# Kernel optimization log

Measured on AMD Instinct MI355X. Metric: run time of the kernel, lower is better.

Reference implementation:

```python
import jax, jax.numpy as jnp
import numpy as np

H = 16      # num_attention_heads
D = 64      # attention_head_size
HID = H * D # hidden_size = 1024
N = 1024    # seq_len == max_len
K = 1024    # position_buckets == att_span (K >= N so un-clamped indices stay in range)
EPS = 1e-7  # layer_norm_eps


def setup_inputs() -> dict:
    key = jax.random.key(0)
    ks = jax.random.split(key, 12)

    def w(k, shape):
        return jax.random.normal(k, shape, dtype=jnp.float32) * 0.02

    return {
        "hidden_states": jax.random.normal(ks[0], (1, N, HID), dtype=jnp.float32),
        "rel_embeddings": jax.random.normal(ks[1], (2 * K, HID), dtype=jnp.float32),
        "Wq": w(ks[2], (HID, HID)), "bq": jnp.zeros((HID,), jnp.float32),
        "Wk": w(ks[3], (HID, HID)), "bk": jnp.zeros((HID,), jnp.float32),
        "Wv": w(ks[4], (HID, HID)), "bv": jnp.zeros((HID,), jnp.float32),
        "Wpk": w(ks[5], (HID, HID)), "bpk": jnp.zeros((HID,), jnp.float32),
        "Wpq": w(ks[6], (HID, HID)), "bpq": jnp.zeros((HID,), jnp.float32),
        "Wo": w(ks[7], (HID, HID)), "bo": jnp.zeros((HID,), jnp.float32),
        "ln_g": jnp.ones((HID,), jnp.float32),
        "ln_b": jnp.zeros((HID,), jnp.float32),
    }


def _heads(x):
    # (L, HID) -> (H, L, D)   (batch size is 1, matching the baked-in id offsets)
    L = x.shape[0]
    return x.reshape(L, H, D).transpose(1, 0, 2)


def reference(hidden_states, rel_embeddings, Wq, bq, Wk, bk, Wv, bv,
              Wpk, bpk, Wpq, bpq, Wo, bo, ln_g, ln_b):
    hs = hidden_states[0]                       # (N, HID)
    q = _heads(hs @ Wq.T + bq)                  # (H, N, D)
    k = _heads(hs @ Wk.T + bk)                  # (H, N, D)
    v = _heads(hs @ Wv.T + bv)                  # (H, N, D)

    scale = jnp.sqrt(jnp.asarray(D * 3, jnp.float32))  # scale_factor = 1 + c2p + p2c = 3
    scores = jnp.einsum('hid,hjd->hij', q, k) / scale  # (H, N, N)

    pos_k = _heads(rel_embeddings @ Wpk.T + bpk)       # (H, 2K, D)
    pos_q = _heads(rel_embeddings @ Wpq.T + bpq)       # (H, 2K, D)

    rows = jnp.arange(N)[:, None]                      # (N, 1)
    # ids[i, j] = (i - j) + K  (no clamp in the original; valid since K >= N)
    idx = K + jnp.arange(N)[:, None] - jnp.arange(N)[None, :]  # (N, N)

    # c2p: gather c2p_att[h, i, K + i - j]
    c2p_att = jnp.einsum('hid,hkd->hik', q, pos_k)     # (H, N, 2K)
    c2p = c2p_att[:, rows, idx]                        # (H, N, N)

    # p2c: gather p2c_att[h, i, K + j - i], then transpose last two dims
    p2c_att = jnp.einsum('hid,hkd->hik', k, pos_q)     # (H, N, 2K)
    p2c = jnp.swapaxes(p2c_att[:, rows, idx.T], -1, -2)  # (H, N, N)

    scores = scores + (c2p + p2c) / scale
    attn = jax.nn.softmax(scores, axis=-1)             # (H, N, N)

    ctx = jnp.einsum('hij,hjd->hid', attn, v)          # (H, N, D)
    ctx = ctx.transpose(1, 0, 2).reshape(1, N, HID)    # (1, N, HID)

    # DebertaV2SelfOutput: dense + residual LayerNorm
    out = ctx @ Wo.T + bo
    x = out + hidden_states
    mu = jnp.mean(x, axis=-1, keepdims=True)
    var = jnp.mean(jnp.square(x - mu), axis=-1, keepdims=True)
    return ((x - mu) / jnp.sqrt(var + EPS)) * ln_g + ln_b
```

## Files before the change

### kernel.cpp

```cpp
#include <hip/hip_runtime.h>
#include <stdint.h>

#define HID 1024
#define NSEQ 1024
#define KREL 1024
#define NHEAD 16
#define DHEAD 64

typedef __attribute__((ext_vector_type(8))) short bhalf8;
typedef __attribute__((ext_vector_type(4))) float floatx4;

__device__ inline uint16_t f2bf(float f) {
  union { float f; uint32_t u; } c; c.f = f;
  uint32_t u = c.u;
  return (uint16_t)((u + 0x7fffu + ((u >> 16) & 1u)) >> 16);
}
__device__ inline uint32_t pkbf(float a, float b) {
  union { float f; uint32_t u; } x, y; x.f = a; y.f = b;
#if __has_builtin(__builtin_amdgcn_perm)
  return __builtin_amdgcn_perm(x.u + 0x8000u, y.u + 0x8000u, 0x03020706u);
#else
  return ((x.u + 0x8000u) >> 16) | ((y.u + 0x8000u) & 0xffff0000u);
#endif
}
// ... 21 lines not shown
  const uint16_t* W[5];
  const float* bias[5];
  uint16_t* C[5];
  int trans[5];
};
__global__ __launch_bounds__(256) void proj_gemm(ProjArgs pa) {
  __shared__ uint16_t a_s[2][128 * 40];
  __shared__ uint16_t b_s[2][128 * 40];
  int bidx = blockIdx.x;
  int xcd = bidx & 7, idx = bidx >> 3;
  int g = xcd * 7 + (idx >> 3);
  int nt = idx & 7;
  int z, mt;
  if (g < 24) { z = g >> 3; mt = g & 7; }
  else { int g2 = g - 24; z = 3 + (g2 >> 4); mt = g2 & 15; }
  const uint16_t* A = pa.A[z];
  const uint16_t* W = pa.W[z];
  int i0 = mt * 128, n0 = nt * 128;

  int t = threadIdx.x;
  int lane = t & 63, w = t >> 6;
  int fm = lane & 15, kq = lane >> 4;
  int wm = (w >> 1) * 64, wn = (w & 1) * 64;

  int ra = t >> 1, ca = (t & 1) * 16;
  const uint16_t* Ap = A + (size_t)(i0 + ra) * HID + ca;
  const uint16_t* Wp = W + (size_t)(n0 + ra) * HID + ca;

  floatx4 acc[4][4] = {};

  uint4 ua0 = *(const uint4*)(Ap);
  uint4 ua1 = *(const uint4*)(Ap + 8);
  uint4 ub0 = *(const uint4*)(Wp);
  uint4 ub1 = *(const uint4*)(Wp + 8);
  *(uint4*)(&a_s[0][ra * 40 + ca]) = ua0;
  *(uint4*)(&a_s[0][ra * 40 + ca + 8]) = ua1;
  *(uint4*)(&b_s[0][ra * 40 + ca]) = ub0;
  *(uint4*)(&b_s[0][ra * 40 + ca + 8]) = ub1;

  for (int kt = 0; kt < 32; ++kt) {
    __syncthreads();
    int cur = kt & 1;
    if (kt < 31) {
      int ko = (kt + 1) * 32;
      ua0 = *(const uint4*)(Ap + ko);
      ua1 = *(const uint4*)(Ap + ko + 8);
      ub0 = *(const uint4*)(Wp + ko);
      ub1 = *(const uint4*)(Wp + ko + 8);
    }
    const uint16_t* as = &a_s[cur][0];
    const uint16_t* bs = &b_s[cur][0];
    bhalf8 af[4], bf[4];
#pragma unroll
    for (int m2 = 0; m2 < 4; ++m2)
      af[m2] = *(bhalf8*)(as + (wm + m2 * 16 + fm) * 40 + kq * 8);
#pragma unroll
    for (int n2 = 0; n2 < 4; ++n2)
      bf[n2] = *(bhalf8*)(bs + (wn + n2 * 16 + fm) * 40 + kq * 8);
#pragma unroll
    for (int m2 = 0; m2 < 4; ++m2)
#pragma unroll
      for (int n2 = 0; n2 < 4; ++n2)
        acc[m2][n2] = __builtin_amdgcn_mfma_f32_16x16x32_bf16(af[m2], bf[n2], acc[m2][n2], 0, 0, 0);
    if (kt < 31) {
      int nxt = cur ^ 1;
      *(uint4*)(&a_s[nxt][ra * 40 + ca]) = ua0;
      *(uint4*)(&a_s[nxt][ra * 40 + ca + 8]) = ua1;
      *(uint4*)(&b_s[nxt][ra * 40 + ca]) = ub0;
      *(uint4*)(&b_s[nxt][ra * 40 + ca + 8]) = ub1;
    }
  }

  const float* bias = pa.bias[z];
  uint16_t* C = pa.C[z];
  int tr = pa.trans[z];
#pragma unroll
  for (int m2 = 0; m2 < 4; ++m2) {
    int rowb = i0 + wm + m2 * 16 + kq * 4;
#pragma unroll
    for (int n2 = 0; n2 < 4; ++n2) {
      int col = n0 + wn + n2 * 16 + fm;
      float bv = bias[col];
      floatx4 v = acc[m2][n2];
      if (tr) {
        uint2 p = { pkbf(v[0] + bv, v[1] + bv), pkbf(v[2] + bv, v[3] + bv) };
        *(uint2*)(C + (size_t)col * NSEQ + rowb) = p;
      } else {
#pragma unroll
        for (int r = 0; r < 4; ++r)
          C[(size_t)(rowb + r) * HID + col] = f2bf(v[r] + bv);
      }
    }
  }
}

__global__ __launch_bounds__(256) void out_gemm(const uint16_t* __restrict__ Abf,
                                                const uint16_t* __restrict__ W,
                                                const float* __restrict__ bias,
                                                float* __restrict__ C) {
  __shared__ uint16_t a_s[2][64 * 40];
  __shared__ uint16_t b_s[2][64 * 40];
  int bidx = blockIdx.x;
  int i0 = (bidx >> 4) * 64, n0 = (bidx & 15) * 64;
  int t = threadIdx.x;
  int lane = t & 63, w = t >> 6;
  int fm = lane & 15, kq = lane >> 4;
  int wm = (w >> 1) * 32, wn = (w & 1) * 32;
  int ra = t >> 2, ca = (t & 3) * 8;
  const uint16_t* Ap = Abf + (size_t)(i0 + ra) * HID + ca;
  const uint16_t* Wp = W + (size_t)(n0 + ra) * HID + ca;
  floatx4 acc00 = {0,0,0,0}, acc01 = {0,0,0,0}, acc10 = {0,0,0,0}, acc11 = {0,0,0,0};
  uint4 ua = *(const uint4*)(Ap);
  uint4 ub = *(const uint4*)(Wp);
  *(uint4*)(&a_s[0][ra * 40 + ca]) = ua;
  *(uint4*)(&b_s[0][ra * 40 + ca]) = ub;
  for (int kt = 0; kt < 32; ++kt) {
    __syncthreads();
    int cur = kt & 1;
    if (kt < 31) {
      int ko = (kt + 1) * 32;
      ua = *(const uint4*)(Ap + ko);
      ub = *(const uint4*)(Wp + ko);
    }
    const uint16_t* as = &a_s[cur][0];
    const uint16_t* bs = &b_s[cur][0];
    bhalf8 a0 = *(bhalf8*)(as + (wm + fm) * 40 + kq * 8);
    bhalf8 a1 = *(bhalf8*)(as + (wm + 16 + fm) * 40 + kq * 8);
    bhalf8 b0 = *(bhalf8*)(bs + (wn + fm) * 40 + kq * 8);
    bhalf8 b1 = *(bhalf8*)(bs + (wn + 16 + fm) * 40 + kq * 8);
    acc00 = __builtin_amdgcn_mfma_f32_16x16x32_bf16(a0, b0, acc00, 0, 0, 0);
    acc01 = __builtin_amdgcn_mfma_f32_16x16x32_bf16(a0, b1, acc01, 0, 0, 0);
    acc10 = __builtin_amdgcn_mfma_f32_16x16x32_bf16(a1, b0, acc10, 0, 0, 0);
    acc11 = __builtin_amdgcn_mfma_f32_16x16x32_bf16(a1, b1, acc11, 0, 0, 0);
    if (kt < 31) {
      int nxt = cur ^ 1;
      *(uint4*)(&a_s[nxt][ra * 40 + ca]) = ua;
      *(uint4*)(&b_s[nxt][ra * 40 + ca]) = ub;
    }
  }
  int rb0 = kq * 4;
#define EPO(ACC, SM, SN)                                                   \
  {                                                                        \
    int rowb = i0 + wm + (SM)*16 + rb0;                                    \
    int col = n0 + wn + (SN)*16 + fm;                                      \
    float bv_ = bias[col];                                                 \
    _Pragma("unroll")                                                      \
    for (int rr = 0; rr < 4; ++rr)                                         \
      C[(size_t)(rowb + rr) * HID + col] = ACC[rr] + bv_;                  \
  }
  EPO(acc00, 0, 0) EPO(acc01, 0, 1) EPO(acc10, 1, 0) EPO(acc11, 1, 1)
#undef EPO
}

__global__ __launch_bounds__(256) void attn_kernel(const uint16_t* __restrict__ qg,
                                                   const uint16_t* __restrict__ kg,
                                                   const uint16_t* __restrict__ vtg,
                                                   const uint16_t* __restrict__ pkg,
                                                   const uint16_t* __restrict__ pqg,
                                                   uint16_t* __restrict__ ctx) {
  const float RSCALE = 0.07216878364870323f;
  __shared__ uint16_t Qs[32][72];
  __shared__ uint16_t Ks[32][72];
  __shared__ uint16_t Vt[64][40];
  __shared__ uint16_t PKw[64][72];
  __shared__ uint16_t PQw[64][72];
  __shared__ float C2P[32][68];
  __shared__ float P2C[32][68];
  __shared__ float Sqk[32][36];
  __shared__ uint16_t Pbf[32][40];
  __shared__ float m_sm[32], l_sm[32], al_sm[32];

  int t = threadIdx.x;
  int lane = t & 63, w = t >> 6;
  int fm = lane & 15;
  int kq = lane >> 4;

  int b = blockIdx.x;
  int xcd = b & 7, slot = b >> 3;
  int h = xcd * 2 + (slot & 1);
  int i0 = (slot >> 1) * 32;
  int cb = h * DHEAD;

  {
    int r = t >> 3, chq = (t & 7) * 8;
    *(uint4*)(&Qs[r][chq]) = *(const uint4*)(qg + (size_t)(i0 + r) * HID + cb + chq);
  }
  if (t < 32) { m_sm[t] = -1e30f; l_sm[t] = 0.f; }

  floatx4 opv0 = {0,0,0,0}, opv1 = {0,0,0,0};
  int wn = w * 16;
  int smt = w >> 1, snt = w & 1;
  int i2 = t >> 3, jj = t & 7;

  int pr = t >> 3, pch = (t & 7) * 8;
  int rV = t >> 2, cV = (t & 3) * 8;
  const uint16_t* kb = kg + cb + pch;
  const uint16_t* vb = vtg + (size_t)(cb + rV) * HID + cV;
  const uint16_t* pkb = pkg + cb + pch;
  const uint16_t* pqb = pqg + cb + pch;

  uint4 rk, rv, rpk0, rpq0;
  {
    int rbase0 = KREL + i0 - 31;
    rk = *(const uint4*)(kb);
    rv = *(const uint4*)(vb);
    int rg0 = rbase0 + pr;
    int rg1 = rg0 + 32; if (rg1 > 2047) rg1 = 2047;
    rpk0 = *(const uint4*)(pkb + (size_t)rg0 * HID);
    uint4 rpk1 = *(const uint4*)(pkb + (size_t)rg1 * HID);
    rpq0 = *(const uint4*)(pqb + (size_t)rg0 * HID);
    uint4 rpq1 = *(const uint4*)(pqb + (size_t)rg1 * HID);
    int prow = rg0 & 63;
    *(uint4*)(&Ks[pr][pch]) = rk;
    *(uint4*)(&Vt[rV][cV]) = rv;
    *(uint4*)(&PKw[prow][pch]) = rpk0;
    *(uint4*)(&PQw[prow][pch]) = rpq0;
    *(uint4*)(&PKw[(prow + 32) & 63][pch]) = rpk1;
    *(uint4*)(&PQw[(prow + 32) & 63][pch]) = rpq1;
  }
  __syncthreads();
  {
    int rbn = KREL + i0 - 63;
    rk = *(const uint4*)(kb + (size_t)(32 + pr) * HID);
    rv = *(const uint4*)(vb + 32);
    rpk0 = *(const uint4*)(pkb + (size_t)(rbn + pr) * HID);
    rpq0 = *(const uint4*)(pqb + (size_t)(rbn + pr) * HID);
  }

  for (int jt = 0; jt < NSEQ / 32; ++jt) {
    int rbase = KREL + i0 - jt * 32 - 31;

    {
      const uint16_t* Asrc = (w < 2) ? &Qs[0][0] : &Ks[0][0];
      const uint16_t* Bsrc = (w < 2) ? &PKw[0][0] : &PQw[0][0];
      float* Cdst = (w < 2) ? &C2P[0][0] : &P2C[0][0];
      int ntb = (w & 1) * 2;
#pragma unroll
      for (int mt = 0; mt < 2; ++mt) {
        bhalf8 a0 = *(bhalf8*)(Asrc + (mt * 16 + fm) * 72 + kq * 8);
        bhalf8 a1 = *(bhalf8*)(Asrc + (mt * 16 + fm) * 72 + kq * 8 + 32);
#pragma unroll
        for (int nt = ntb; nt < ntb + 2; ++nt) {
          int wrow = (rbase + nt * 16 + fm) & 63;
          bhalf8 b0 = *(bhalf8*)(Bsrc + wrow * 72 + kq * 8);
          bhalf8 b1 = *(bhalf8*)(Bsrc + wrow * 72 + kq * 8 + 32);
          floatx4 acc = {0,0,0,0};
          acc = __builtin_amdgcn_mfma_f32_16x16x32_bf16(a0, b0, acc, 0, 0, 0);
          acc = __builtin_amdgcn_mfma_f32_16x16x32_bf16(a1, b1, acc, 0, 0, 0);
#pragma unroll
          for (int r = 0; r < 4; ++r)
            Cdst[(mt * 16 + kq * 4 + r) * 68 + nt * 16 + fm] = acc[r];
        }
      }
      bhalf8 qa0 = *(bhalf8*)(&Qs[smt * 16 + fm][kq * 8]);
      bhalf8 qa1 = *(bhalf8*)(&Qs[smt * 16 + fm][kq * 8 + 32]);
      bhalf8 kb0 = *(bhalf8*)(&Ks[snt * 16 + fm][kq * 8]);
      bhalf8 kb1 = *(bhalf8*)(&Ks[snt * 16 + fm][kq * 8 + 32]);
      floatx4 sacc = {0,0,0,0};
      sacc = __builtin_amdgcn_mfma_f32_16x16x32_bf16(qa0, kb0, sacc, 0, 0, 0);
      sacc = __builtin_amdgcn_mfma_f32_16x16x32_bf16(qa1, kb1, sacc, 0, 0, 0);
#pragma unroll
      for (int r = 0; r < 4; ++r)
        Sqk[smt * 16 + kq * 4 + r][snt * 16 + fm] = sacc[r];
    }
    __syncthreads();

    if (jt < 31) {
      int prow = (rbase - 32 + pr) & 63;
      *(uint4*)(&Ks[pr][pch]) = rk;
      *(uint4*)(&PKw[prow][pch]) = rpk0;
      *(uint4*)(&PQw[prow][pch]) = rpq0;
    }

    {
      float sv[4];
#pragma unroll
      for (int q = 0; q < 4; ++q) {
        int j = jj + 8 * q;
        int rr = i2 - j + 31;
        sv[q] = (Sqk[i2][j] + C2P[i2][rr] + P2C[j][rr]) * RSCALE;
      }
      float mx = fmaxf(fmaxf(sv[0], sv[1]), fmaxf(sv[2], sv[3]));
      mx = fmaxf(mx, __shfl_xor(mx, 1));
      mx = fmaxf(mx, __shfl_xor(mx, 2));
      mx = fmaxf(mx, __shfl_xor(mx, 4));
      float m_old = m_sm[i2];
      float m_new = fmaxf(m_old, mx);
      float al = __expf(m_old - m_new);
      float ts = 0.f;
#pragma unroll
      for (int q = 0; q < 4; ++q) {
        float e = __expf(sv[q] - m_new);
        Pbf[i2][jj + 8 * q] = f2bf(e);
        ts += e;
      }
      ts += __shfl_xor(ts, 1);
      ts += __shfl_xor(ts, 2);
      ts += __shfl_xor(ts, 4);
      if (jj == 0) { m_sm[i2] = m_new; l_sm[i2] = l_sm[i2] * al + ts; al_sm[i2] = al; }
    }

    if (jt < 30) {
      int j0 = (jt + 2) * 32;
      int rbn = KREL + i0 - j0 - 31;
      rk = *(const uint4*)(kb + (size_t)(j0 + pr) * HID);
      rpk0 = *(const uint4*)(pkb + (size_t)(rbn + pr) * HID);
      rpq0 = *(const uint4*)(pqb + (size_t)(rbn + pr) * HID);
    }
    __syncthreads();

    {
#pragma unroll
      for (int r = 0; r < 4; ++r) {
        opv0[r] *= al_sm[kq * 4 + r];
        opv1[r] *= al_sm[16 + kq * 4 + r];
      }
      bhalf8 vbf = *(bhalf8*)(&Vt[wn + fm][kq * 8]);
      bhalf8 pa0 = *(bhalf8*)(&Pbf[fm][kq * 8]);
      bhalf8 pa1 = *(bhalf8*)(&Pbf[16 + fm][kq * 8]);
      opv0 = __builtin_amdgcn_mfma_f32_16x16x32_bf16(pa0, vbf, opv0, 0, 0, 0);
      opv1 = __builtin_amdgcn_mfma_f32_16x16x32_bf16(pa1, vbf, opv1, 0, 0, 0);
      if (jt < 31) *(uint4*)(&Vt[rV][cV]) = rv;
      if (jt < 30) rv = *(const uint4*)(vb + (jt + 2) * 32);
    }
  }

#pragma unroll
  for (int r = 0; r < 4; ++r) {
    int ia = kq * 4 + r, ib = 16 + kq * 4 + r;
    float la = 1.0f / l_sm[ia], lb = 1.0f / l_sm[ib];
    ctx[(size_t)(i0 + ia) * HID + cb + wn + fm] = f2bf(opv0[r] * la);
    ctx[(size_t)(i0 + ib) * HID + cb + wn + fm] = f2bf(opv1[r] * lb);
  }
}

__global__ __launch_bounds__(256) void ln_kernel(const float* __restrict__ xin,
                                                 const float* __restrict__ hs,
                                                 const float* __restrict__ g,
                                                 const float* __restrict__ b,
                                                 float* __restrict__ y) {
  int row = blockIdx.x, t = threadIdx.x;
  int c = t * 4;
  float4 a = *(const float4*)(xin + (size_t)row * HID + c);
  float4 hv = *(const float4*)(hs + (size_t)row * HID + c);
  float x0 = a.x + hv.x, x1 = a.y + hv.y, x2 = a.z + hv.z, x3 = a.w + hv.w;
  float s = x0 + x1 + x2 + x3;
  float sq = x0 * x0 + x1 * x1 + x2 * x2 + x3 * x3;
  for (int off = 32; off; off >>= 1) {
    s += __shfl_xor(s, off);
    sq += __shfl_xor(sq, off);
  }
  __shared__ float rs[4], rq[4];
  int w = t >> 6, lane = t & 63;
  if (lane == 0) { rs[w] = s; rq[w] = sq; }
  __syncthreads();
  s = rs[0] + rs[1] + rs[2] + rs[3];
  sq = rq[0] + rq[1] + rq[2] + rq[3];
  float mu = s * (1.0f / HID);
  float var = sq * (1.0f / HID) - mu * mu;
  float rstd = rsqrtf(var + 1e-7f);
  float4 gg = *(const float4*)(g + c);
  float4 bb = *(const float4*)(b + c);
  float4 out;
  out.x = (x0 - mu) * rstd * gg.x + bb.x;
  out.y = (x1 - mu) * rstd * gg.y + bb.y;
  out.z = (x2 - mu) * rstd * gg.z + bb.z;
  out.w = (x3 - mu) * rstd * gg.w + bb.w;
  *(float4*)(y + (size_t)row * HID + c) = out;
}

extern "C" void kernel_launch(void* const* d_in, const int* in_sizes, int n_in,
                              void* d_out, int out_size, void* d_ws, size_t ws_size,
                              hipStream_t stream) {
  const float* hs  = (const float*)d_in[0];
  const float* rel = (const float*)d_in[1];
  const float* Wq  = (const float*)d_in[2];  const float* bq  = (const float*)d_in[3];
  const float* Wk  = (const float*)d_in[4];  const float* bk  = (const float*)d_in[5];
  const float* Wv  = (const float*)d_in[6];  const float* bv  = (const float*)d_in[7];
  const float* Wpk = (const float*)d_in[8];  const float* bpk = (const float*)d_in[9];
  const float* Wpq = (const float*)d_in[10]; const float* bpq = (const float*)d_in[11];
  const float* Wo  = (const float*)d_in[12]; const float* bo  = (const float*)d_in[13];
  const float* lng = (const float*)d_in[14]; const float* lnb = (const float*)d_in[15];

  char* ws = (char*)d_ws;
  const size_t MB = 1024 * 1024;
  uint16_t* q_bf   = (uint16_t*)(ws + 0 * MB);
  uint16_t* k_bf   = (uint16_t*)(ws + 2 * MB);
  uint16_t* vt_bf  = (uint16_t*)(ws + 4 * MB);
  uint16_t* pk_bf  = (uint16_t*)(ws + 6 * MB);
  uint16_t* pq_bf  = (uint16_t*)(ws + 10 * MB);
  uint16_t* ctx_bf = (uint16_t*)(ws + 14 * MB);
  float*    out_f  = (float*)   (ws + 16 * MB);
  uint16_t* hs_bf  = (uint16_t*)(ws + 20 * MB);
  uint16_t* rel_bf = (uint16_t*)(ws + 22 * MB);
  uint16_t* Wq_bf  = (uint16_t*)(ws + 26 * MB);
  uint16_t* Wk_bf  = (uint16_t*)(ws + 28 * MB);
  uint16_t* Wv_bf  = (uint16_t*)(ws + 30 * MB);
  uint16_t* Wpk_bf = (uint16_t*)(ws + 32 * MB);
  uint16_t* Wpq_bf = (uint16_t*)(ws + 34 * MB);
  uint16_t* Wo_bf  = (uint16_t*)(ws + 36 * MB);

  dim3 blk(256);

  Cast8 c8;
  c8.src[0] = hs;  c8.dst[0] = hs_bf;  c8.n[0] = 1024 * 1024;
  c8.src[1] = rel; c8.dst[1] = rel_bf; c8.n[1] = 2048 * 1024;
  c8.src[2] = Wq;  c8.dst[2] = Wq_bf;  c8.n[2] = 1024 * 1024;
  c8.src[3] = Wk;  c8.dst[3] = Wk_bf;  c8.n[3] = 1024 * 1024;
  c8.src[4] = Wv;  c8.dst[4] = Wv_bf;  c8.n[4] = 1024 * 1024;
  c8.src[5] = Wpk; c8.dst[5] = Wpk_bf; c8.n[5] = 1024 * 1024;
  c8.src[6] = Wpq; c8.dst[6] = Wpq_bf; c8.n[6] = 1024 * 1024;
  c8.src[7] = Wo;  c8.dst[7] = Wo_bf;  c8.n[7] = 1024 * 1024;
  cast8_kernel<<<dim3(1024, 8), blk, 0, stream>>>(c8);

  ProjArgs pa;
  pa.A[0] = hs_bf;  pa.A[1] = hs_bf;  pa.A[2] = hs_bf;  pa.A[3] = rel_bf; pa.A[4] = rel_bf;
  pa.W[0] = Wq_bf;  pa.W[1] = Wk_bf;  pa.W[2] = Wv_bf;  pa.W[3] = Wpk_bf; pa.W[4] = Wpq_bf;
  pa.bias[0] = bq;  pa.bias[1] = bk;  pa.bias[2] = bv;  pa.bias[3] = bpk; pa.bias[4] = bpq;
  pa.C[0] = q_bf; pa.C[1] = k_bf; pa.C[2] = vt_bf; pa.C[3] = pk_bf; pa.C[4] = pq_bf;
  pa.trans[0] = 0; pa.trans[1] = 0; pa.trans[2] = 1; pa.trans[3] = 0; pa.trans[4] = 0;
  proj_gemm<<<dim3(448), blk, 0, stream>>>(pa);

  attn_kernel<<<dim3(512), blk, 0, stream>>>(q_bf, k_bf, vt_bf, pk_bf, pq_bf, ctx_bf);

  out_gemm<<<dim3(256), blk, 0, stream>>>(ctx_bf, Wo_bf, bo, out_f);

  ln_kernel<<<dim3(1024), blk, 0, stream>>>(out_f, hs, lng, lnb, (float*)d_out);
}
```

Before: 201.2 us.

## Double attention block to 512 threads and split per-tile work across eight waves

The attention kernel now runs 512 threads per block instead of 256. The C2P/P2C MFMA tiles, the QK tile, the softmax rows and the PV accumulation are redistributed across eight waves. Global loads are split between two thread halves, and V gets a double-buffered shared tile. The aim is more parallelism per block and less serial work per wave in each j-tile. The cost is larger blocks, a bit more shared memory and possibly lower occupancy, with the same number of barriers per iteration.

Result: slower. 210.6 us (+4.7%).

```diff
diff --git a/kernel.cpp b/kernel.cpp
--- a/kernel.cpp
+++ b/kernel.cpp
@@ -197,7 +197,7 @@
 #undef EPO
 }
 
-__global__ __launch_bounds__(256) void attn_kernel(const uint16_t* __restrict__ qg,
+__global__ __launch_bounds__(512) void attn_kernel(const uint16_t* __restrict__ qg,
                                                    const uint16_t* __restrict__ kg,
                                                    const uint16_t* __restrict__ vtg,
                                                    const uint16_t* __restrict__ pkg,
@@ -206,7 +206,7 @@
   const float RSCALE = 0.07216878364870323f;
   __shared__ uint16_t Qs[32][72];
   __shared__ uint16_t Ks[32][72];
-  __shared__ uint16_t Vt[64][40];
+  __shared__ uint16_t Vt[2][64][40];
   __shared__ uint16_t PKw[64][72];
   __shared__ uint16_t PQw[64][72];
   __shared__ float C2P[32][68];
@@ -226,156 +226,170 @@
   int i0 = (slot >> 1) * 32;
   int cb = h * DHEAD;
 
-  {
-    int r = t >> 3, chq = (t & 7) * 8;
-    *(uint4*)(&Qs[r][chq]) = *(const uint4*)(qg + (size_t)(i0 + r) * HID + cb + chq);
-  }
-  if (t < 32) { m_sm[t] = -1e30f; l_sm[t] = 0.f; }
-
-  floatx4 opv0 = {0,0,0,0}, opv1 = {0,0,0,0};
-  int wn = w * 16;
-  int smt = w >> 1, snt = w & 1;
-  int i2 = t >> 3, jj = t & 7;
-
-  int pr = t >> 3, pch = (t & 7) * 8;
-  int rV = t >> 2, cV = (t & 3) * 8;
+  int ts = t & 255;
+  int grpB = t >> 8;
+  int pr = ts >> 3, pch = (ts & 7) * 8;
+  int rV = ts >> 2, cV = (ts & 3) * 8;
   const uint16_t* kb = kg + cb + pch;
   const uint16_t* vb = vtg + (size_t)(cb + rV) * HID + cV;
   const uint16_t* pkb = pkg + cb + pch;
   const uint16_t* pqb = pqg + cb + pch;
 
+  if (t < 32) { m_sm[t] = -1e30f; l_sm[t] = 0.f; }
+
+  floatx4 opv = {0, 0, 0, 0};
+
   uint4 rk, rv, rpk0, rpq0;
   {
     int rbase0 = KREL + i0 - 31;
-    rk = *(const uint4*)(kb);
-    rv = *(const uint4*)(vb);
     int rg0 = rbase0 + pr;
     int rg1 = rg0 + 32; if (rg1 > 2047) rg1 = 2047;
-    rpk0 = *(const uint4*)(pkb + (size_t)rg0 * HID);
-    uint4 rpk1 = *(const uint4*)(pkb + (size_t)rg1 * HID);
-    rpq0 = *(const uint4*)(pqb + (size_t)rg0 * HID);
-    uint4 rpq1 = *(const uint4*)(pqb + (size_t)rg1 * HID);
     int prow = rg0 & 63;
-    *(uint4*)(&Ks[pr][pch]) = rk;
-    *(uint4*)(&Vt[rV][cV]) = rv;
-    *(uint4*)(&PKw[prow][pch]) = rpk0;
-    *(uint4*)(&PQw[prow][pch]) = rpq0;
-    *(uint4*)(&PKw[(prow + 32) & 63][pch]) = rpk1;
-    *(uint4*)(&PQw[(prow + 32) & 63][pch]) = rpq1;
+    if (!grpB) {
+      *(uint4*)(&Qs[pr][pch]) = *(const uint4*)(qg + (size_t)(i0 + pr) * HID + cb + pch);
+      rk = *(const uint4*)(kb);
+      rpk0 = *(const uint4*)(pkb + (size_t)rg0 * HID);
+      uint4 rpk1 = *(const uint4*)(pkb + (size_t)rg1 * HID);
+      *(uint4*)(&Ks[pr][pch]) = rk;
+      *(uint4*)(&PKw[prow][pch]) = rpk0;
+      *(uint4*)(&PKw[(prow + 32) & 63][pch]) = rpk1;
+    } else {
+      rv = *(const uint4*)(vb);
+      rpq0 = *(const uint4*)(pqb + (size_t)rg0 * HID);
+      uint4 rpq1 = *(const uint4*)(pqb + (size_t)rg1 * HID);
+      *(uint4*)(&Vt[0][rV][cV]) = rv;
+      *(uint4*)(&PQw[prow][pch]) = rpq0;
+      *(uint4*)(&PQw[(prow + 32) & 63][pch]) = rpq1;
+    }
   }
   __syncthreads();
   {
     int rbn = KREL + i0 - 63;
-    rk = *(const uint4*)(kb + (size_t)(32 + pr) * HID);
-    rv = *(const uint4*)(vb + 32);
-    rpk0 = *(const uint4*)(pkb + (size_t)(rbn + pr) * HID);
-    rpq0 = *(const uint4*)(pqb + (size_t)(rbn + pr) * HID);
-  }
+    if (!grpB) {
+      rk = *(const uint4*)(kb + (size_t)(32 + pr) * HID);
+      rpk0 = *(const uint4*)(pkb + (size_t)(rbn + pr) * HID);
+    } else {
+      rv = *(const uint4*)(vb + 32);
+      rpq0 = *(const uint4*)(pqb + (size_t)(rbn + pr) * HID);
+    }
+  }
+
+  int isP2C = w >> 2;
+  int w2 = w & 3;
+  int mt1 = w2 >> 1;
+  int ntb = (w2 & 1) * 2;
+  int doSqk = ((w & 1) == 0);
+  int sq = w >> 1;
+  int smt = sq >> 1, snt = sq & 1;
+  int i2 = t >> 4, jj = t & 15;
+  int rblk = (w & 1) * 16, cblk = (w >> 1) * 16;
 
   for (int jt = 0; jt < NSEQ / 32; ++jt) {
     int rbase = KREL + i0 - jt * 32 - 31;
+    int cur = jt & 1;
 
     {
-      const uint16_t* Asrc = (w < 2) ? &Qs[0][0] : &Ks[0][0];
-      const uint16_t* Bsrc = (w < 2) ? &PKw[0][0] : &PQw[0][0];
-      float* Cdst = (w < 2) ? &C2P[0][0] : &P2C[0][0];
-      int ntb = (w & 1) * 2;
-#pragma unroll
-      for (int mt = 0; mt < 2; ++mt) {
-        bhalf8 a0 = *(bhalf8*)(Asrc + (mt * 16 + fm) * 72 + kq * 8);
-        bhalf8 a1 = *(bhalf8*)(Asrc + (mt * 16 + fm) * 72 + kq * 8 + 32);
-#pragma unroll
-        for (int nt = ntb; nt < ntb + 2; ++nt) {
-          int wrow = (rbase + nt * 16 + fm) & 63;
-          bhalf8 b0 = *(bhalf8*)(Bsrc + wrow * 72 + kq * 8);
-          bhalf8 b1 = *(bhalf8*)(Bsrc + wrow * 72 + kq * 8 + 32);
-          floatx4 acc = {0,0,0,0};
-          acc = __builtin_amdgcn_mfma_f32_16x16x32_bf16(a0, b0, acc, 0, 0, 0);
-          acc = __builtin_amdgcn_mfma_f32_16x16x32_bf16(a1, b1, acc, 0, 0, 0);
-#pragma unroll
-          for (int r = 0; r < 4; ++r)
-            Cdst[(mt * 16 + kq * 4 + r) * 68 + nt * 16 + fm] = acc[r];
-        }
-      }
-      bhalf8 qa0 = *(bhalf8*)(&Qs[smt * 16 + fm][kq * 8]);
-      bhalf8 qa1 = *(bhalf8*)(&Qs[smt * 16 + fm][kq * 8 + 32]);
-      bhalf8 kb0 = *(bhalf8*)(&Ks[snt * 16 + fm][kq * 8]);
-      bhalf8 kb1 = *(bhalf8*)(&Ks[snt * 16 + fm][kq * 8 + 32]);
-      floatx4 sacc = {0,0,0,0};
-      sacc = __builtin_amdgcn_mfma_f32_16x16x32_bf16(qa0, kb0, sacc, 0, 0, 0);
-      sacc = __builtin_amdgcn_mfma_f32_16x16x32_bf16(qa1, kb1, sacc, 0, 0, 0);
-#pragma unroll
-      for (int r = 0; r < 4; ++r)
-        Sqk[smt * 16 + kq * 4 + r][snt * 16 + fm] = sacc[r];
+      const uint16_t* Asrc = isP2C ? &Ks[0][0] : &Qs[0][0];
+      const uint16_t* Bsrc = isP2C ? &PQw[0][0] : &PKw[0][0];
+      float* Cdst = isP2C ? &P2C[0][0] : &C2P[0][0];
+      bhalf8 a0 = *(bhalf8*)(Asrc + (mt1 * 16 + fm) * 72 + kq * 8);
+      bhalf8 a1 = *(bhalf8*)(Asrc + (mt1 * 16 + fm) * 72 + kq * 8 + 32);
+#pragma unroll
+      for (int nt = ntb; nt < ntb + 2; ++nt) {
+        int wrow = (rbase + nt * 16 + fm) & 63;
+        bhalf8 b0 = *(bhalf8*)(Bsrc + wrow * 72 + kq * 8);
+        bhalf8 b1 = *(bhalf8*)(Bsrc + wrow * 72 + kq * 8 + 32);
+        floatx4 acc = {0, 0, 0, 0};
+        acc = __builtin_amdgcn_mfma_f32_16x16x32_bf16(a0, b0, acc, 0, 0, 0);
+        acc = __builtin_amdgcn_mfma_f32_16x16x32_bf16(a1, b1, acc, 0, 0, 0);
+#pragma unroll
+        for (int r = 0; r < 4; ++r)
+          Cdst[(mt1 * 16 + kq * 4 + r) * 68 + nt * 16 + fm] = acc[r];
+      }
+      if (doSqk) {
+        bhalf8 qa0 = *(bhalf8*)(&Qs[smt * 16 + fm][kq * 8]);
+        bhalf8 qa1 = *(bhalf8*)(&Qs[smt * 16 + fm][kq * 8 + 32]);
+        bhalf8 kb0 = *(bhalf8*)(&Ks[snt * 16 + fm][kq * 8]);
+        bhalf8 kb1 = *(bhalf8*)(&Ks[snt * 16 + fm][kq * 8 + 32]);
+        floatx4 sacc = {0, 0, 0, 0};
+        sacc = __builtin_amdgcn_mfma_f32_16x16x32_bf16(qa0, kb0, sacc, 0, 0, 0);
+        sacc = __builtin_amdgcn_mfma_f32_16x16x32_bf16(qa1, kb1, sacc, 0, 0, 0);
+#pragma unroll
+        for (int r = 0; r < 4; ++r)
+          Sqk[smt * 16 + kq * 4 + r][snt * 16 + fm] = sacc[r];
+      }
     }
     __syncthreads();
 
     if (jt < 31) {
       int prow = (rbase - 32 + pr) & 63;
-      *(uint4*)(&Ks[pr][pch]) = rk;
-      *(uint4*)(&PKw[prow][pch]) = rpk0;
-      *(uint4*)(&PQw[prow][pch]) = rpq0;
+      if (!grpB) {
+        *(uint4*)(&Ks[pr][pch]) = rk;
+        *(uint4*)(&PKw[prow][pch]) = rpk0;
+      } else {
+        *(uint4*)(&PQw[prow][pch]) = rpq0;
+        *(uint4*)(&Vt[cur ^ 1][rV][cV]) = rv;
+      }
     }
 
     {
-      float sv[4];
-#pragma unroll
-      for (int q = 0; q < 4; ++q) {
-        int j = jj + 8 * q;
+      float sv[2];
+#pragma unroll
+      for (int q = 0; q < 2; ++q) {
+        int j = jj + 16 * q;
         int rr = i2 - j + 31;
         sv[q] = (Sqk[i2][j] + C2P[i2][rr] + P2C[j][rr]) * RSCALE;
       }
-      float mx = fmaxf(fmaxf(sv[0], sv[1]), fmaxf(sv[2], sv[3]));
+      float mx = fmaxf(sv[0], sv[1]);
       mx = fmaxf(mx, __shfl_xor(mx, 1));
       mx = fmaxf(mx, __shfl_xor(mx, 2));
       mx = fmaxf(mx, __shfl_xor(mx, 4));
+      mx = fmaxf(mx, __shfl_xor(mx, 8));
       float m_old = m_sm[i2];
       float m_new = fmaxf(m_old, mx);
       float al = __expf(m_old - m_new);
-      float ts = 0.f;
-#pragma unroll
-      for (int q = 0; q < 4; ++q) {
+      float tsum = 0.f;
+#pragma unroll
+      for (int q = 0; q < 2; ++q) {
         float e = __expf(sv[q] - m_new);
-        Pbf[i2][jj + 8 * q] = f2bf(e);
-        ts += e;
-      }
-      ts += __shfl_xor(ts, 1);
-      ts += __shfl_xor(ts, 2);
-      ts += __shfl_xor(ts, 4);
-      if (jj == 0) { m_sm[i2] = m_new; l_sm[i2] = l_sm[i2] * al + ts; al_sm[i2] = al; }
+        Pbf[i2][jj + 16 * q] = f2bf(e);
+        tsum += e;
+      }
+      tsum += __shfl_xor(tsum, 1);
+      tsum += __shfl_xor(tsum, 2);
+      tsum += __shfl_xor(tsum, 4);
+      tsum += __shfl_xor(tsum, 8);
+      if (jj == 0) { m_sm[i2] = m_new; l_sm[i2] = l_sm[i2] * al + tsum; al_sm[i2] = al; }
     }
 
     if (jt < 30) {
       int j0 = (jt + 2) * 32;
       int rbn = KREL + i0 - j0 - 31;
-      rk = *(const uint4*)(kb + (size_t)(j0 + pr) * HID);
-      rpk0 = *(const uint4*)(pkb + (size_t)(rbn + pr) * HID);
-      rpq0 = *(const uint4*)(pqb + (size_t)(rbn + pr) * HID);
+      if (!grpB) {
+        rk = *(const uint4*)(kb + (size_t)(j0 + pr) * HID);
+        rpk0 = *(const uint4*)(pkb + (size_t)(rbn + pr) * HID);
+      } else {
+        rv = *(const uint4*)(vb + j0);
+        rpq0 = *(const uint4*)(pqb + (size_t)(rbn + pr) * HID);
+      }
     }
     __syncthreads();
 
     {
 #pragma unroll
-      for (int r = 0; r < 4; ++r) {
-        opv0[r] *= al_sm[kq * 4 + r];
-        opv1[r] *= al_sm[16 + kq * 4 + r];
-      }
-      bhalf8 vbf = *(bhalf8*)(&Vt[wn + fm][kq * 8]);
-      bhalf8 pa0 = *(bhalf8*)(&Pbf[fm][kq * 8]);
-      bhalf8 pa1 = *(bhalf8*)(&Pbf[16 + fm][kq * 8]);
-      opv0 = __builtin_amdgcn_mfma_f32_16x16x32_bf16(pa0, vbf, opv0, 0, 0, 0);
-      opv1 = __builtin_amdgcn_mfma_f32_16x16x32_bf16(pa1, vbf, opv1, 0, 0, 0);
-      if (jt < 31) *(uint4*)(&Vt[rV][cV]) = rv;
-      if (jt < 30) rv = *(const uint4*)(vb + (jt + 2) * 32);
+      for (int r = 0; r < 4; ++r)
+        opv[r] *= al_sm[rblk + kq * 4 + r];
+      bhalf8 vbf = *(bhalf8*)(&Vt[cur][cblk + fm][kq * 8]);
+      bhalf8 pa = *(bhalf8*)(&Pbf[rblk + fm][kq * 8]);
+      opv = __builtin_amdgcn_mfma_f32_16x16x32_bf16(pa, vbf, opv, 0, 0, 0);
     }
   }
 
 #pragma unroll
   for (int r = 0; r < 4; ++r) {
-    int ia = kq * 4 + r, ib = 16 + kq * 4 + r;
-    float la = 1.0f / l_sm[ia], lb = 1.0f / l_sm[ib];
-    ctx[(size_t)(i0 + ia) * HID + cb + wn + fm] = f2bf(opv0[r] * la);
-    ctx[(size_t)(i0 + ib) * HID + cb + wn + fm] = f2bf(opv1[r] * lb);
+    int ia = rblk + kq * 4 + r;
+    float la = 1.0f / l_sm[ia];
+    ctx[(size_t)(i0 + ia) * HID + cb + cblk + fm] = f2bf(opv[r] * la);
   }
 }
 
@@ -466,7 +480,7 @@
   pa.trans[0] = 0; pa.trans[1] = 0; pa.trans[2] = 1; pa.trans[3] = 0; pa.trans[4] = 0;
   proj_gemm<<<dim3(448), blk, 0, stream>>>(pa);
 
-  attn_kernel<<<dim3(512), blk, 0, stream>>>(q_bf, k_bf, vt_bf, pk_bf, pq_bf, ctx_bf);
+  attn_kernel<<<dim3(512), dim3(512), 0, stream>>>(q_bf, k_bf, vt_bf, pk_bf, pq_bf, ctx_bf);
 
   out_gemm<<<dim3(256), blk, 0, stream>>>(ctx_bf, Wo_bf, bo, out_f);
 
```

## Software-pipeline attention score MFMAs one tile ahead with double-buffered score tiles

Applied to the files above, without the earlier changes.

The Sqk, C2P and P2C score tiles are now double-buffered, and a prologue computes the first tile before the loop. Each iteration reads the current scores into registers, then issues the next tile's MFMAs into the other buffer before running softmax. This lets the score matrix work overlap the softmax and PV stages. The K/PK/PQ prefetch now runs one tile further ahead, and there is an extra barrier at the end of each iteration. Shared-memory use grows by about 26 KB, which may lower occupancy.

After: 199.5 us. No clear change (-0.8%).

```diff
diff --git a/kernel.cpp b/kernel.cpp
--- a/kernel.cpp
+++ b/kernel.cpp
@@ -209,9 +209,9 @@
   __shared__ uint16_t Vt[64][40];
   __shared__ uint16_t PKw[64][72];
   __shared__ uint16_t PQw[64][72];
-  __shared__ float C2P[32][68];
-  __shared__ float P2C[32][68];
-  __shared__ float Sqk[32][36];
+  __shared__ float C2P[2][32][68];
+  __shared__ float P2C[2][32][68];
+  __shared__ float Sqk[2][32][36];
   __shared__ uint16_t Pbf[32][40];
   __shared__ float m_sm[32], l_sm[32], al_sm[32];
 
@@ -265,20 +265,82 @@
   }
   __syncthreads();
   {
-    int rbn = KREL + i0 - 63;
+    int rb1 = KREL + i0 - 63;
     rk = *(const uint4*)(kb + (size_t)(32 + pr) * HID);
     rv = *(const uint4*)(vb + 32);
-    rpk0 = *(const uint4*)(pkb + (size_t)(rbn + pr) * HID);
-    rpq0 = *(const uint4*)(pqb + (size_t)(rbn + pr) * HID);
-  }
+    rpk0 = *(const uint4*)(pkb + (size_t)(rb1 + pr) * HID);
+    rpq0 = *(const uint4*)(pqb + (size_t)(rb1 + pr) * HID);
+  }
+  {
+    int rbase = KREL + i0 - 31;
+    const uint16_t* Asrc = (w < 2) ? &Qs[0][0] : &Ks[0][0];
+    const uint16_t* Bsrc = (w < 2) ? &PKw[0][0] : &PQw[0][0];
+    float* Cdst = (w < 2) ? &C2P[0][0][0] : &P2C[0][0][0];
+    int ntb = (w & 1) * 2;
+#pragma unroll
+    for (int mt = 0; mt < 2; ++mt) {
+      bhalf8 a0 = *(bhalf8*)(Asrc + (mt * 16 + fm) * 72 + kq * 8);
+      bhalf8 a1 = *(bhalf8*)(Asrc + (mt * 16 + fm) * 72 + kq * 8 + 32);
+#pragma unroll
+      for (int nt = ntb; nt < ntb + 2; ++nt) {
+        int wrow = (rbase + nt * 16 + fm) & 63;
+        bhalf8 b0 = *(bhalf8*)(Bsrc + wrow * 72 + kq * 8);
+        bhalf8 b1 = *(bhalf8*)(Bsrc + wrow * 72 + kq * 8 + 32);
+        floatx4 acc = {0,0,0,0};
+        acc = __builtin_amdgcn_mfma_f32_16x16x32_bf16(a0, b0, acc, 0, 0, 0);
+        acc = __builtin_amdgcn_mfma_f32_16x16x32_bf16(a1, b1, acc, 0, 0, 0);
+#pragma unroll
+        for (int r = 0; r < 4; ++r)
+          Cdst[(mt * 16 + kq * 4 + r) * 68 + nt * 16 + fm] = acc[r];
+      }
+    }
+    bhalf8 qa0 = *(bhalf8*)(&Qs[smt * 16 + fm][kq * 8]);
+    bhalf8 qa1 = *(bhalf8*)(&Qs[smt * 16 + fm][kq * 8 + 32]);
+    bhalf8 kb0 = *(bhalf8*)(&Ks[snt * 16 + fm][kq * 8]);
+    bhalf8 kb1 = *(bhalf8*)(&Ks[snt * 16 + fm][kq * 8 + 32]);
+    floatx4 sacc = {0,0,0,0};
+    sacc = __builtin_amdgcn_mfma_f32_16x16x32_bf16(qa0, kb0, sacc, 0, 0, 0);
+    sacc = __builtin_amdgcn_mfma_f32_16x16x32_bf16(qa1, kb1, sacc, 0, 0, 0);
+#pragma unroll
+    for (int r = 0; r < 4; ++r)
+      Sqk[0][smt * 16 + kq * 4 + r][snt * 16 + fm] = sacc[r];
+  }
+  __syncthreads();
+  {
+    int rb1 = KREL + i0 - 63;
+    int prow = (rb1 + pr) & 63;
+    *(uint4*)(&Ks[pr][pch]) = rk;
+    *(uint4*)(&PKw[prow][pch]) = rpk0;
+    *(uint4*)(&PQw[prow][pch]) = rpq0;
+    int rb2 = KREL + i0 - 95;
+    rk = *(const uint4*)(kb + (size_t)(64 + pr) * HID);
+    rpk0 = *(const uint4*)(pkb + (size_t)(rb2 + pr) * HID);
+    rpq0 = *(const uint4*)(pqb + (size_t)(rb2 + pr) * HID);
+  }
+  __syncthreads();
 
   for (int jt = 0; jt < NSEQ / 32; ++jt) {
-    int rbase = KREL + i0 - jt * 32 - 31;
-
-    {
+    int cur = jt & 1;
+    const float* SQKc = &Sqk[cur][0][0];
+    const float* C2Pc = &C2P[cur][0][0];
+    const float* P2Cc = &P2C[cur][0][0];
+
+    float t_sqk[4], t_c2p[4], t_p2c[4];
+#pragma unroll
+    for (int q = 0; q < 4; ++q) {
+      int j = jj + 8 * q;
+      int rr = i2 - j + 31;
+      t_sqk[q] = SQKc[i2 * 36 + j];
+      t_c2p[q] = C2Pc[i2 * 68 + rr];
+      t_p2c[q] = P2Cc[j * 68 + rr];
+    }
+
+    if (jt < 31) {
+      int rbase = KREL + i0 - (jt + 1) * 32 - 31;
+      int bi = cur ^ 1;
       const uint16_t* Asrc = (w < 2) ? &Qs[0][0] : &Ks[0][0];
       const uint16_t* Bsrc = (w < 2) ? &PKw[0][0] : &PQw[0][0];
-      float* Cdst = (w < 2) ? &C2P[0][0] : &P2C[0][0];
+      float* Cdst = (w < 2) ? &C2P[bi][0][0] : &P2C[bi][0][0];
       int ntb = (w & 1) * 2;
 #pragma unroll
       for (int mt = 0; mt < 2; ++mt) {
@@ -306,25 +368,14 @@
       sacc = __builtin_amdgcn_mfma_f32_16x16x32_bf16(qa1, kb1, sacc, 0, 0, 0);
 #pragma unroll
       for (int r = 0; r < 4; ++r)
-        Sqk[smt * 16 + kq * 4 + r][snt * 16 + fm] = sacc[r];
-    }
-    __syncthreads();
-
-    if (jt < 31) {
-      int prow = (rbase - 32 + pr) & 63;
-      *(uint4*)(&Ks[pr][pch]) = rk;
-      *(uint4*)(&PKw[prow][pch]) = rpk0;
-      *(uint4*)(&PQw[prow][pch]) = rpq0;
+        Sqk[bi][smt * 16 + kq * 4 + r][snt * 16 + fm] = sacc[r];
     }
 
     {
       float sv[4];
 #pragma unroll
-      for (int q = 0; q < 4; ++q) {
-        int j = jj + 8 * q;
-        int rr = i2 - j + 31;
-        sv[q] = (Sqk[i2][j] + C2P[i2][rr] + P2C[j][rr]) * RSCALE;
-      }
+      for (int q = 0; q < 4; ++q)
+        sv[q] = (t_sqk[q] + t_c2p[q] + t_p2c[q]) * RSCALE;
       float mx = fmaxf(fmaxf(sv[0], sv[1]), fmaxf(sv[2], sv[3]));
       mx = fmaxf(mx, __shfl_xor(mx, 1));
       mx = fmaxf(mx, __shfl_xor(mx, 2));
@@ -343,14 +394,6 @@
       ts += __shfl_xor(ts, 2);
       ts += __shfl_xor(ts, 4);
       if (jj == 0) { m_sm[i2] = m_new; l_sm[i2] = l_sm[i2] * al + ts; al_sm[i2] = al; }
-    }
-
-    if (jt < 30) {
-      int j0 = (jt + 2) * 32;
-      int rbn = KREL + i0 - j0 - 31;
-      rk = *(const uint4*)(kb + (size_t)(j0 + pr) * HID);
-      rpk0 = *(const uint4*)(pkb + (size_t)(rbn + pr) * HID);
-      rpq0 = *(const uint4*)(pqb + (size_t)(rbn + pr) * HID);
     }
     __syncthreads();
 
@@ -368,6 +411,21 @@
       if (jt < 31) *(uint4*)(&Vt[rV][cV]) = rv;
       if (jt < 30) rv = *(const uint4*)(vb + (jt + 2) * 32);
     }
+    if (jt < 30) {
+      int rb2 = KREL + i0 - (jt + 2) * 32 - 31;
+      int prow = (rb2 + pr) & 63;
+      *(uint4*)(&Ks[pr][pch]) = rk;
+      *(uint4*)(&PKw[prow][pch]) = rpk0;
+      *(uint4*)(&PQw[prow][pch]) = rpq0;
+    }
+    if (jt < 29) {
+      int j0 = (jt + 3) * 32;
+      int rb3 = KREL + i0 - j0 - 31;
+      rk = *(const uint4*)(kb + (size_t)(j0 + pr) * HID);
+      rpk0 = *(const uint4*)(pkb + (size_t)(rb3 + pr) * HID);
+      rpq0 = *(const uint4*)(pqb + (size_t)(rb3 + pr) * HID);
+    }
+    __syncthreads();
   }
 
 #pragma unroll
```

## Software-pipeline attention stage1 with double-buffered score tiles and direct-register pos loads

Applied to the files above, without the earlier changes.

Restructures the attention loop so the QK, c2p and p2c MFMA products for tile jt+1 are computed into a second buffer while softmax runs on tile jt. The PKw/PQw shared-memory windows are removed, and positional B-fragments are loaded straight from global memory into registers. The c2p result is written pre-shifted so softmax can read it with vector loads. This aims to overlap compute stages and cut LDS traffic, at the cost of more registers, an extra barrier per iteration and redundant global loads of positional rows.

After: 200.4 us. About the same (-0.4%).

```diff
diff --git a/kernel.cpp b/kernel.cpp
--- a/kernel.cpp
+++ b/kernel.cpp
@@ -207,11 +207,9 @@
   __shared__ uint16_t Qs[32][72];
   __shared__ uint16_t Ks[32][72];
   __shared__ uint16_t Vt[64][40];
-  __shared__ uint16_t PKw[64][72];
-  __shared__ uint16_t PQw[64][72];
-  __shared__ float C2P[32][68];
-  __shared__ float P2C[32][68];
-  __shared__ float Sqk[32][36];
+  __shared__ float C2Ps[2][32][68];
+  __shared__ float P2C[2][32][68];
+  __shared__ float Sqk[2][32][36];
   __shared__ uint16_t Pbf[32][40];
   __shared__ float m_sm[32], l_sm[32], al_sm[32];
 
@@ -235,130 +233,152 @@
   floatx4 opv0 = {0,0,0,0}, opv1 = {0,0,0,0};
   int wn = w * 16;
   int smt = w >> 1, snt = w & 1;
-  int i2 = t >> 3, jj = t & 7;
+  int i2 = t >> 3, jj4 = (t & 7) * 4;
 
   int pr = t >> 3, pch = (t & 7) * 8;
   int rV = t >> 2, cV = (t & 3) * 8;
   const uint16_t* kb = kg + cb + pch;
   const uint16_t* vb = vtg + (size_t)(cb + rV) * HID + cV;
-  const uint16_t* pkb = pkg + cb + pch;
-  const uint16_t* pqb = pqg + cb + pch;
-
-  uint4 rk, rv, rpk0, rpq0;
+
+  int ntb = (w & 1) * 2;
+  int brow_f = ntb * 16 + fm;
+  const uint16_t* bgp = ((w < 2) ? pkg : pqg) + cb + kq * 8;
+  int cbase = 31 - brow_f + kq * 4;
+
+  uint4 rk, rv;
+  bhalf8 nbA0, nbA1, nbB0, nbB1;
+
+#define STAGE1(BUF, BA0, BA1, BB0, BB1)                                          \
+  do {                                                                           \
+    if (w < 2) {                                                                 \
+      _Pragma("unroll")                                                          \
+      for (int mt = 0; mt < 2; ++mt) {                                           \
+        bhalf8 a0 = *(bhalf8*)(&Qs[mt * 16 + fm][kq * 8]);                       \
+        bhalf8 a1 = *(bhalf8*)(&Qs[mt * 16 + fm][kq * 8 + 32]);                  \
+        floatx4 ac0 = {0,0,0,0}, ac1 = {0,0,0,0};                                \
+        ac0 = __builtin_amdgcn_mfma_f32_16x16x32_bf16(a0, BA0, ac0, 0, 0, 0);    \
+        ac0 = __builtin_amdgcn_mfma_f32_16x16x32_bf16(a1, BA1, ac0, 0, 0, 0);    \
+        ac1 = __builtin_amdgcn_mfma_f32_16x16x32_bf16(a0, BB0, ac1, 0, 0, 0);    \
+        ac1 = __builtin_amdgcn_mfma_f32_16x16x32_bf16(a1, BB1, ac1, 0, 0, 0);    \
+        _Pragma("unroll")                                                        \
+        for (int r = 0; r < 4; ++r) {                                            \
+          int i = mt * 16 + kq * 4 + r;                                          \
+          C2Ps[BUF][i][(cbase + mt * 16 + r) & 63] = ac0[r];                     \
+          C2Ps[BUF][i][(cbase + mt * 16 + r - 16) & 63] = ac1[r];                \
+        }                                                                        \
+      }                                                                          \
+    } else {                                                                     \
+      _Pragma("unroll")                                                          \
+      for (int mt = 0; mt < 2; ++mt) {                                           \
+        bhalf8 a0 = *(bhalf8*)(&Ks[mt * 16 + fm][kq * 8]);                       \
+        bhalf8 a1 = *(bhalf8*)(&Ks[mt * 16 + fm][kq * 8 + 32]);                  \
+        floatx4 ac0 = {0,0,0,0}, ac1 = {0,0,0,0};                                \
+        ac0 = __builtin_amdgcn_mfma_f32_16x16x32_bf16(a0, BA0, ac0, 0, 0, 0);    \
+        ac0 = __builtin_amdgcn_mfma_f32_16x16x32_bf16(a1, BA1, ac0, 0, 0, 0);    \
+        ac1 = __builtin_amdgcn_mfma_f32_16x16x32_bf16(a0, BB0, ac1, 0, 0, 0);    \
+        ac1 = __builtin_amdgcn_mfma_f32_16x16x32_bf16(a1, BB1, ac1, 0, 0, 0);    \
+        _Pragma("unroll")                                                        \
+        for (int r = 0; r < 4; ++r) {                                            \
+          int jr = mt * 16 + kq * 4 + r;                                         \
+          P2C[BUF][jr][brow_f] = ac0[r];                                         \
+          P2C[BUF][jr][brow_f + 16] = ac1[r];                                    \
+        }                                                                        \
+      }                                                                          \
+    }                                                                            \
+    {                                                                            \
+      bhalf8 qa0 = *(bhalf8*)(&Qs[smt * 16 + fm][kq * 8]);                       \
+      bhalf8 qa1 = *(bhalf8*)(&Qs[smt * 16 + fm][kq * 8 + 32]);                  \
+      bhalf8 kb0 = *(bhalf8*)(&Ks[snt * 16 + fm][kq * 8]);                       \
+      bhalf8 kb1 = *(bhalf8*)(&Ks[snt * 16 + fm][kq * 8 + 32]);                  \
+      floatx4 sacc = {0,0,0,0};                                                  \
+      sacc = __builtin_amdgcn_mfma_f32_16x16x32_bf16(qa0, kb0, sacc, 0, 0, 0);   \
+      sacc = __builtin_amdgcn_mfma_f32_16x16x32_bf16(qa1, kb1, sacc, 0, 0, 0);   \
+      _Pragma("unroll")                                                          \
+      for (int r = 0; r < 4; ++r)                                                \
+        Sqk[BUF][smt * 16 + kq * 4 + r][snt * 16 + fm] = sacc[r];                \
+    }                                                                            \
+  } while (0)
+
+  rk = *(const uint4*)(kb);
+  rv = *(const uint4*)(vb);
+  *(uint4*)(&Ks[pr][pch]) = rk;
+  *(uint4*)(&Vt[rV][cV]) = rv;
+  __syncthreads();
+  rk = *(const uint4*)(kb + (size_t)(32 + pr) * HID);
+  rv = *(const uint4*)(vb + 32);
   {
-    int rbase0 = KREL + i0 - 31;
-    rk = *(const uint4*)(kb);
-    rv = *(const uint4*)(vb);
-    int rg0 = rbase0 + pr;
-    int rg1 = rg0 + 32; if (rg1 > 2047) rg1 = 2047;
-    rpk0 = *(const uint4*)(pkb + (size_t)rg0 * HID);
-    uint4 rpk1 = *(const uint4*)(pkb + (size_t)rg1 * HID);
-    rpq0 = *(const uint4*)(pqb + (size_t)rg0 * HID);
-    uint4 rpq1 = *(const uint4*)(pqb + (size_t)rg1 * HID);
-    int prow = rg0 & 63;
-    *(uint4*)(&Ks[pr][pch]) = rk;
-    *(uint4*)(&Vt[rV][cV]) = rv;
-    *(uint4*)(&PKw[prow][pch]) = rpk0;
-    *(uint4*)(&PQw[prow][pch]) = rpq0;
-    *(uint4*)(&PKw[(prow + 32) & 63][pch]) = rpk1;
-    *(uint4*)(&PQw[(prow + 32) & 63][pch]) = rpq1;
+    int rbase = KREL + i0 - 31;
+    int r0 = rbase + brow_f;      if (r0 > 2047) r0 = 2047;
+    int r1 = rbase + brow_f + 16; if (r1 > 2047) r1 = 2047;
+    bhalf8 tA0 = *(const bhalf8*)(bgp + ((size_t)r0 << 10));
+    bhalf8 tA1 = *(const bhalf8*)(bgp + ((size_t)r0 << 10) + 32);
+    bhalf8 tB0 = *(const bhalf8*)(bgp + ((size_t)r1 << 10));
+    bhalf8 tB1 = *(const bhalf8*)(bgp + ((size_t)r1 << 10) + 32);
+    STAGE1(0, tA0, tA1, tB0, tB1);
   }
   __syncthreads();
   {
-    int rbn = KREL + i0 - 63;
-    rk = *(const uint4*)(kb + (size_t)(32 + pr) * HID);
-    rv = *(const uint4*)(vb + 32);
-    rpk0 = *(const uint4*)(pkb + (size_t)(rbn + pr) * HID);
-    rpq0 = *(const uint4*)(pqb + (size_t)(rbn + pr) * HID);
-  }
+    *(uint4*)(&Ks[pr][pch]) = rk;
+    rk = *(const uint4*)(kb + (size_t)(64 + pr) * HID);
+    int rb1 = KREL + i0 - 63;
+    int r0 = rb1 + brow_f;
+    nbA0 = *(const bhalf8*)(bgp + ((size_t)r0 << 10));
+    nbA1 = *(const bhalf8*)(bgp + ((size_t)r0 << 10) + 32);
+    nbB0 = *(const bhalf8*)(bgp + ((size_t)(r0 + 16) << 10));
+    nbB1 = *(const bhalf8*)(bgp + ((size_t)(r0 + 16) << 10) + 32);
+  }
+  __syncthreads();
 
   for (int jt = 0; jt < NSEQ / 32; ++jt) {
-    int rbase = KREL + i0 - jt * 32 - 31;
+    int cur = jt & 1;
+
+    float4 v_sqk = *(const float4*)(&Sqk[cur][i2][jj4]);
+    float4 v_c2p = *(const float4*)(&C2Ps[cur][i2][jj4]);
+    float p0 = P2C[cur][jj4 + 0][i2 - jj4 + 31];
+    float p1 = P2C[cur][jj4 + 1][i2 - jj4 + 30];
+    float p2 = P2C[cur][jj4 + 2][i2 - jj4 + 29];
+    float p3 = P2C[cur][jj4 + 3][i2 - jj4 + 28];
+
+    if (jt < 31) {
+      int bi = cur ^ 1;
+      STAGE1(bi, nbA0, nbA1, nbB0, nbB1);
+    }
 
     {
-      const uint16_t* Asrc = (w < 2) ? &Qs[0][0] : &Ks[0][0];
-      const uint16_t* Bsrc = (w < 2) ? &PKw[0][0] : &PQw[0][0];
-      float* Cdst = (w < 2) ? &C2P[0][0] : &P2C[0][0];
-      int ntb = (w & 1) * 2;
-#pragma unroll
-      for (int mt = 0; mt < 2; ++mt) {
-        bhalf8 a0 = *(bhalf8*)(Asrc + (mt * 16 + fm) * 72 + kq * 8);
-        bhalf8 a1 = *(bhalf8*)(Asrc + (mt * 16 + fm) * 72 + kq * 8 + 32);
-#pragma unroll
-        for (int nt = ntb; nt < ntb + 2; ++nt) {
-          int wrow = (rbase + nt * 16 + fm) & 63;
-          bhalf8 b0 = *(bhalf8*)(Bsrc + wrow * 72 + kq * 8);
-          bhalf8 b1 = *(bhalf8*)(Bsrc + wrow * 72 + kq * 8 + 32);
-          floatx4 acc = {0,0,0,0};
-          acc = __builtin_amdgcn_mfma_f32_16x16x32_bf16(a0, b0, acc, 0, 0, 0);
-          acc = __builtin_amdgcn_mfma_f32_16x16x32_bf16(a1, b1, acc, 0, 0, 0);
-#pragma unroll
-          for (int r = 0; r < 4; ++r)
-            Cdst[(mt * 16 + kq * 4 + r) * 68 + nt * 16 + fm] = acc[r];
-        }
-      }
-      bhalf8 qa0 = *(bhalf8*)(&Qs[smt * 16 + fm][kq * 8]);
-      bhalf8 qa1 = *(bhalf8*)(&Qs[smt * 16 + fm][kq * 8 + 32]);
-      bhalf8 kb0 = *(bhalf8*)(&Ks[snt * 16 + fm][kq * 8]);
-      bhalf8 kb1 = *(bhalf8*)(&Ks[snt * 16 + fm][kq * 8 + 32]);
-      floatx4 sacc = {0,0,0,0};
-      sacc = __builtin_amdgcn_mfma_f32_16x16x32_bf16(qa0, kb0, sacc, 0, 0, 0);
-      sacc = __builtin_amdgcn_mfma_f32_16x16x32_bf16(qa1, kb1, sacc, 0, 0, 0);
-#pragma unroll
-      for (int r = 0; r < 4; ++r)
-        Sqk[smt * 16 + kq * 4 + r][snt * 16 + fm] = sacc[r];
-    }
-    __syncthreads();
-
-    if (jt < 31) {
-      int prow = (rbase - 32 + pr) & 63;
-      *(uint4*)(&Ks[pr][pch]) = rk;
-      *(uint4*)(&PKw[prow][pch]) = rpk0;
-      *(uint4*)(&PQw[prow][pch]) = rpq0;
-    }
-
-    {
-      float sv[4];
-#pragma unroll
-      for (int q = 0; q < 4; ++q) {
-        int j = jj + 8 * q;
-        int rr = i2 - j + 31;
-        sv[q] = (Sqk[i2][j] + C2P[i2][rr] + P2C[j][rr]) * RSCALE;
-      }
-      float mx = fmaxf(fmaxf(sv[0], sv[1]), fmaxf(sv[2], sv[3]));
+      float sv0 = (v_sqk.x + v_c2p.x + p0) * RSCALE;
+      float sv1 = (v_sqk.y + v_c2p.y + p1) * RSCALE;
+      float sv2 = (v_sqk.z + v_c2p.z + p2) * RSCALE;
+      float sv3 = (v_sqk.w + v_c2p.w + p3) * RSCALE;
+      float mx = fmaxf(fmaxf(sv0, sv1), fmaxf(sv2, sv3));
       mx = fmaxf(mx, __shfl_xor(mx, 1));
       mx = fmaxf(mx, __shfl_xor(mx, 2));
       mx = fmaxf(mx, __shfl_xor(mx, 4));
       float m_old = m_sm[i2];
       float m_new = fmaxf(m_old, mx);
       float al = __expf(m_old - m_new);
-      float ts = 0.f;
-#pragma unroll
-      for (int q = 0; q < 4; ++q) {
-        float e = __expf(sv[q] - m_new);
-        Pbf[i2][jj + 8 * q] = f2bf(e);
-        ts += e;
-      }
+      float e0 = __expf(sv0 - m_new);
+      float e1 = __expf(sv1 - m_new);
+      float e2 = __expf(sv2 - m_new);
+      float e3 = __expf(sv3 - m_new);
+      uint2 pk2v;
+      pk2v.x = (uint32_t)f2bf(e0) | ((uint32_t)f2bf(e1) << 16);
+      pk2v.y = (uint32_t)f2bf(e2) | ((uint32_t)f2bf(e3) << 16);
+      *(uint2*)(&Pbf[i2][jj4]) = pk2v;
+      float ts = (e0 + e1) + (e2 + e3);
       ts += __shfl_xor(ts, 1);
       ts += __shfl_xor(ts, 2);
       ts += __shfl_xor(ts, 4);
-      if (jj == 0) { m_sm[i2] = m_new; l_sm[i2] = l_sm[i2] * al + ts; al_sm[i2] = al; }
-    }
-
-    if (jt < 30) {
-      int j0 = (jt + 2) * 32;
-      int rbn = KREL + i0 - j0 - 31;
-      rk = *(const uint4*)(kb + (size_t)(j0 + pr) * HID);
-      rpk0 = *(const uint4*)(pkb + (size_t)(rbn + pr) * HID);
-      rpq0 = *(const uint4*)(pqb + (size_t)(rbn + pr) * HID);
+      if (jj4 == 0) { m_sm[i2] = m_new; l_sm[i2] = l_sm[i2] * al + ts; al_sm[i2] = al; }
     }
     __syncthreads();
 
     {
+      floatx4 al0 = *(const floatx4*)(&al_sm[kq * 4]);
+      floatx4 al1 = *(const floatx4*)(&al_sm[16 + kq * 4]);
 #pragma unroll
       for (int r = 0; r < 4; ++r) {
-        opv0[r] *= al_sm[kq * 4 + r];
-        opv1[r] *= al_sm[16 + kq * 4 + r];
+        opv0[r] *= al0[r];
+        opv1[r] *= al1[r];
       }
       bhalf8 vbf = *(bhalf8*)(&Vt[wn + fm][kq * 8]);
       bhalf8 pa0 = *(bhalf8*)(&Pbf[fm][kq * 8]);
@@ -368,14 +388,33 @@
       if (jt < 31) *(uint4*)(&Vt[rV][cV]) = rv;
       if (jt < 30) rv = *(const uint4*)(vb + (jt + 2) * 32);
     }
-  }
-
-#pragma unroll
-  for (int r = 0; r < 4; ++r) {
-    int ia = kq * 4 + r, ib = 16 + kq * 4 + r;
-    float la = 1.0f / l_sm[ia], lb = 1.0f / l_sm[ib];
-    ctx[(size_t)(i0 + ia) * HID + cb + wn + fm] = f2bf(opv0[r] * la);
-    ctx[(size_t)(i0 + ib) * HID + cb + wn + fm] = f2bf(opv1[r] * lb);
+    if (jt < 30) {
+      *(uint4*)(&Ks[pr][pch]) = rk;
+    }
+    if (jt < 29) {
+      rk = *(const uint4*)(kb + (size_t)((jt + 3) * 32 + pr) * HID);
+    }
+    if (jt < 30) {
+      int rb = KREL + i0 - (jt + 2) * 32 - 31;
+      int r0 = rb + brow_f;
+      nbA0 = *(const bhalf8*)(bgp + ((size_t)r0 << 10));
+      nbA1 = *(const bhalf8*)(bgp + ((size_t)r0 << 10) + 32);
+      nbB0 = *(const bhalf8*)(bgp + ((size_t)(r0 + 16) << 10));
+      nbB1 = *(const bhalf8*)(bgp + ((size_t)(r0 + 16) << 10) + 32);
+    }
+    __syncthreads();
+  }
+#undef STAGE1
+
+  {
+    floatx4 l0 = *(const floatx4*)(&l_sm[kq * 4]);
+    floatx4 l1 = *(const floatx4*)(&l_sm[16 + kq * 4]);
+#pragma unroll
+    for (int r = 0; r < 4; ++r) {
+      int ia = kq * 4 + r, ib = 16 + kq * 4 + r;
+      ctx[(size_t)(i0 + ia) * HID + cb + wn + fm] = f2bf(opv0[r] / l0[r]);
+      ctx[(size_t)(i0 + ib) * HID + cb + wn + fm] = f2bf(opv1[r] / l1[r]);
+    }
   }
 }
 
```
